# Kernel tuning notes

Measured on AMD Instinct MI355X. Metric: run time of the kernel, lower is better.

The kernel has to match this reference:

```python
import math
import jax, jax.numpy as jnp
import numpy as np

D, H, L, DFF, V = 512, 8, 6, 2048, 32000
B, S = 2, 2048
PAD = 1


def _layernorm(x, g, b, eps=1e-5):
    m = x.mean(-1, keepdims=True)
    v = ((x - m) ** 2).mean(-1, keepdims=True)
    return (x - m) / jnp.sqrt(v + eps) * g + b


def _mha(qx, kx, w, b, mask, h=H):
    # w: [4, D, D] (q,k,v,out), b: [4, D]; mask broadcastable to [B,1,Sq,Sk]
    bs, sq, d = qx.shape
    dk = d // h
    def proj(x, i):
        return (x @ w[i] + b[i]).reshape(bs, -1, h, dk).transpose(0, 2, 1, 3)
    q, k, v = proj(qx, 0), proj(kx, 1), proj(kx, 2)
    scores = jnp.einsum('bhqd,bhkd->bhqk', q, k) / math.sqrt(dk)
    scores = jnp.where(mask, scores, -jnp.inf)
    attn = jax.nn.softmax(scores, axis=-1)
    out = jnp.einsum('bhqk,bhkd->bhqd', attn, v).transpose(0, 2, 1, 3).reshape(bs, sq, d)
    return out @ w[3] + b[3]


def _ff(x, w1, b1, w2, b2):
    return jax.nn.relu(x @ w1 + b1) @ w2 + b2


def _sinusoidal_pe(max_len, d):
    pos = np.arange(max_len)[:, None].astype(np.float64)
    div = np.exp(np.arange(0, d, 2) * (-math.log(10000.0) / d))
    pe = np.zeros((max_len, d), np.float32)
    pe[:, 0::2] = np.sin(pos * div)
    pe[:, 1::2] = np.cos(pos * div)
    return jnp.asarray(pe[None])  # [1, max_len, d]


def setup_inputs() -> dict:
    key = jax.random.key(0)
    ks = iter(jax.random.split(key, 32))
    def w(shape):
        return jax.random.normal(next(ks), shape, jnp.float32) * 0.02
    inp = {
        'src': jax.random.randint(next(ks), (B, S), 2, V),
        'tgt': jax.random.randint(next(ks), (B, S), 2, V),
        'src_emb': w((V, D)),
        'tgt_emb': w((V, D)),
        'pe': _sinusoidal_pe(S, D),
        'enc_attn_w': w((L, 4, D, D)), 'enc_attn_b': jnp.zeros((L, 4, D)),
        'enc_ff_w1': w((L, D, DFF)), 'enc_ff_b1': jnp.zeros((L, DFF)),
        'enc_ff_w2': w((L, DFF, D)), 'enc_ff_b2': jnp.zeros((L, D)),
        'enc_ln_g': jnp.ones((L, 2, D)), 'enc_ln_b': jnp.zeros((L, 2, D)),
        'dec_self_w': w((L, 4, D, D)), 'dec_self_b': jnp.zeros((L, 4, D)),
        'dec_src_w': w((L, 4, D, D)), 'dec_src_b': jnp.zeros((L, 4, D)),
        'dec_ff_w1': w((L, D, DFF)), 'dec_ff_b1': jnp.zeros((L, DFF)),
        'dec_ff_w2': w((L, DFF, D)), 'dec_ff_b2': jnp.zeros((L, D)),
        'dec_ln_g': jnp.ones((L, 3, D)), 'dec_ln_b': jnp.zeros((L, 3, D)),
        'ln_g': jnp.ones((D,)), 'ln_b': jnp.zeros((D,)),
        'fc_w': w((D, V)), 'fc_b': jnp.zeros((V,)),
    }
    return inp


def reference(src, tgt, src_emb, tgt_emb, pe,
              enc_attn_w, enc_attn_b, enc_ff_w1, enc_ff_b1, enc_ff_w2, enc_ff_b2,
              enc_ln_g, enc_ln_b,
              dec_self_w, dec_self_b, dec_src_w, dec_src_b,
              dec_ff_w1, dec_ff_b1, dec_ff_w2, dec_ff_b2, dec_ln_g, dec_ln_b,
              ln_g, ln_b, fc_w, fc_b):
    s_len, t_len = src.shape[1], tgt.shape[1]
    src_mask = (src != PAD)[:, None, None, :]                      # [B,1,1,Ss]
    tril = jnp.tril(jnp.ones((t_len, t_len), bool))
    tgt_mask = (tgt != PAD)[:, None, None, :] & tril[None, None]   # [B,1,St,St]

    x = src_emb[src] + pe[:, :s_len]
    for l in range(L):
        x2 = _layernorm(x, enc_ln_g[l, 0], enc_ln_b[l, 0])
        x = x + _mha(x2, x2, enc_attn_w[l], enc_attn_b[l], src_mask)
        x2 = _layernorm(x, enc_ln_g[l, 1], enc_ln_b[l, 1])
        x = x + _ff(x2, enc_ff_w1[l], enc_ff_b1[l], enc_ff_w2[l], enc_ff_b2[l])
    memory = x

    y = tgt_emb[tgt] + pe[:, :t_len]
    for l in range(L):
        y2 = _layernorm(y, dec_ln_g[l, 0], dec_ln_b[l, 0])
        y = y + _mha(y2, y2, dec_self_w[l], dec_self_b[l], tgt_mask)
        y2 = _layernorm(y, dec_ln_g[l, 1], dec_ln_b[l, 1])
        y = y + _mha(y2, memory, dec_src_w[l], dec_src_b[l], src_mask)
        y2 = _layernorm(y, dec_ln_g[l, 2], dec_ln_b[l, 2])
        y = y + _ff(y2, dec_ff_w1[l], dec_ff_b1[l], dec_ff_w2[l], dec_ff_b2[l])

    return _layernorm(y, ln_g, ln_b) @ fc_w + fc_b  # [B, St, V]
```

## Files before the change

kernel.cpp:

```cpp
#include <hip/hip_runtime.h>
#include <math.h>

#define D_MODEL 512
#define NHEAD   8
#define NLAYER  6
#define DFF_    2048
#define VOCAB   32000
#define BATCH   2
#define SEQ     2048
#define NTOK    (BATCH*SEQ)
#define PAD_ID  1

typedef __attribute__((ext_vector_type(8))) short s16x8;
typedef __attribute__((ext_vector_type(4))) float f32x4;
typedef unsigned short u16;
typedef unsigned int   u32;
typedef unsigned long long u64;

__device__ __forceinline__ u16 f2bf(float x) {
  u32 u = __builtin_bit_cast(u32, x);
  u += 0x7FFFu + ((u >> 16) & 1u);
  return (u16)(u >> 16);
}

__device__ __forceinline__ float exp2i(float x) {
  float r; asm("v_exp_f32 %0, %1" : "=v"(r) : "v"(x)); return r;
}

__device__ __forceinline__ void gload16(const void* g, void* l) {
  __builtin_amdgcn_global_load_lds(
      (const __attribute__((address_space(1))) u32*)g,
      (__attribute__((address_space(3))) u32*)l, 16, 0, 0);
}

#define CEXP 0.1803368802f

__global__ __launch_bounds__(256) void embed_kernel(
    const int* __restrict__ tok, const float* __restrict__ emb,
    const float* __restrict__ pe, float* __restrict__ out)
{
  const int total = NTOK * D_MODEL;
  for (int i = blockIdx.x * 256 + threadIdx.x; i < total; i += gridDim.x * 256) {
    int t = i >> 9;
    int d = i & 511;
    int s = t & (SEQ - 1);
    out[i] = emb[(size_t)tok[t] * D_MODEL + d] + pe[(size_t)s * D_MODEL + d];
  }
}

__global__ __launch_bounds__(64) void padmask_kernel(
    const int* __restrict__ tok, u64* __restrict__ pm)
{
  int b = blockIdx.y, t = blockIdx.x;
  int lane = threadIdx.x;
  u64 m = __ballot(tok[(size_t)b * SEQ + t * 64 + lane] != PAD_ID);
  if (lane == 0) pm[b * (SEQ / 64) + t] = m;
}

__global__ __launch_bounds__(256) void ln_kernel(
    const float* __restrict__ x, const float* __restrict__ g,
    const float* __restrict__ bb, u16* __restrict__ y)
{
  __shared__ float red[8];
  const size_t row = blockIdx.x;
  const float* xr = x + row * D_MODEL;
  u16* yr = y + row * D_MODEL;
  const int t = threadIdx.x;
  float a0 = xr[t], a1 = xr[t + 256];
  float s = a0 + a1;
  #pragma unroll
  for (int o = 32; o > 0; o >>= 1) s += __shfl_down(s, o, 64);
  int wv = t >> 6, ln = t & 63;
  if (ln == 0) red[wv] = s;
  __syncthreads();
  if (t == 0) red[4] = red[0] + red[1] + red[2] + red[3];
  __syncthreads();
  float mean = red[4] * (1.0f / D_MODEL);
  float d0 = a0 - mean, d1 = a1 - mean;
  float vs = d0 * d0 + d1 * d1;
  #pragma unroll
  for (int o = 32; o > 0; o >>= 1) vs += __shfl_down(vs, o, 64);
  if (ln == 0) red[wv] = vs;
  __syncthreads();
  if (t == 0) red[5] = red[0] + red[1] + red[2] + red[3];
  __syncthreads();
  float inv = rsqrtf(red[5] * (1.0f / D_MODEL) + 1e-5f);
  yr[t]       = f2bf(d0 * inv * g[t]       + bb[t]);
  yr[t + 256] = f2bf(d1 * inv * g[t + 256] + bb[t + 256]);
}

__global__ __launch_bounds__(256) void cvtbf_kernel(
    const float* __restrict__ s, u16* __restrict__ d, int n)
{
  int i = (blockIdx.x * 256 + threadIdx.x) * 8;
  if (i >= n) return;
  float4 a = *(const float4*)&s[i];
  float4 b = *(const float4*)&s[i + 4];
  u32 p0 = (u32)f2bf(a.x) | ((u32)f2bf(a.y) << 16);
  u32 p1 = (u32)f2bf(a.z) | ((u32)f2bf(a.w) << 16);
  u32 p2 = (u32)f2bf(b.x) | ((u32)f2bf(b.y) << 16);
  u32 p3 = (u32)f2bf(b.z) | ((u32)f2bf(b.w) << 16);
  uint4 o; o.x = p0; o.y = p1; o.z = p2; o.w = p3;
  *(uint4*)&d[i] = o;
}

__global__ __launch_bounds__(256) void tconv_kernel(
    const float* __restrict__ src, u16* __restrict__ dst, int K, int N)
{
  __shared__ float tile[64][65];
  const size_t z = blockIdx.z;
  src += z * (size_t)K * N;
  dst += z * (size_t)K * N;
  const int n0 = blockIdx.x * 64, k0 = blockIdx.y * 64;
  const int t = threadIdx.x;
  const int cr = t >> 4, cc = (t & 15) * 4;
  #pragma unroll
  for (int it = 0; it < 4; ++it) {
    int kr = cr + it * 16;
    float4 v = *(const float4*)&src[(size_t)(k0 + kr) * N + n0 + cc];
    tile[kr][cc] = v.x; tile[kr][cc + 1] = v.y; tile[kr][cc + 2] = v.z; tile[kr][cc + 3] = v.w;
  }
  __syncthreads();
  #pragma unroll
  for (int it = 0; it < 4; ++it) {
    int nr = cr + it * 16;
    u32 lo = (u32)f2bf(tile[cc + 0][nr]) | ((u32)f2bf(tile[cc + 1][nr]) << 16);
    u32 hi = (u32)f2bf(tile[cc + 2][nr]) | ((u32)f2bf(tile[cc + 3][nr]) << 16);
    uint2 pk; pk.x = lo; pk.y = hi;
    *(uint2*)&dst[(size_t)(n0 + nr) * K + k0 + cc] = pk;
  }
}

__global__ __launch_bounds__(256) void vtrans_kernel(
    const u16* __restrict__ v, u16* __restrict__ vt)
{
  __shared__ u16 tile[64][65];
  const int bh = blockIdx.z, s0 = blockIdx.x * 64;
  const int b = bh >> 3, h = bh & 7;
  const int t = threadIdx.x;
  const int lr = t >> 3, lc = (t & 7) * 8;
  #pragma unroll
  for (int it = 0; it < 2; ++it) {
    int srow = lr + it * 32;
    s16x8 val = *(const s16x8*)(v + (size_t)(b * SEQ + s0 + srow) * D_MODEL + h * 64 + lc);
    #pragma unroll
    for (int j = 0; j < 8; ++j) tile[srow][lc + j] = (u16)val[j];
  }
  __syncthreads();
  #pragma unroll
  for (int it = 0; it < 2; ++it) {
    int drow = lr + it * 32;
    s16x8 o;
    #pragma unroll
    for (int j = 0; j < 8; ++j) o[j] = (short)tile[lc + j][drow];
    *(s16x8*)(vt + ((size_t)bh * 64 + drow) * SEQ + s0 + lc) = o;
  }
}

template<int MODE, int BM>
__global__ __launch_bounds__(256, 2) void mm_kernel(
    const u16* __restrict__ A, const u16* __restrict__ Wt,
    const float* __restrict__ bias, const float* __restrict__ res,
    void* __restrict__ Cout, int M, int N, int K,
    long long wStride, long long bStride, long long cStride)
{
  constexpr int MI = BM / 32;
  __shared__ u16 As[BM * 64];
  __shared__ u16 Bs[128 * 64];
  const int z = blockIdx.z;
  Wt   += (size_t)z * wStride;
  bias += (size_t)z * bStride;
  const int bm = blockIdx.y * BM, bn = blockIdx.x * 128;
  const int tid = threadIdx.x, lane = tid & 63, w = tid >> 6;
  const int wm = w >> 1, wn = w & 1;
  const int l15 = lane & 15, l4 = lane >> 4;
  const int wrow0 = wm * (BM / 2);
  const u16* aBase = A  + (size_t)bm * K;
  const u16* bBase = Wt + (size_t)bn * K;
  f32x4 acc[MI][4] = {};

  for (int k0 = 0; k0 < K; k0 += 64) {
    #pragma unroll
    for (int i = 0; i < BM / 32; ++i) {
      int lin = i * 256 + tid;
      int r = lin >> 3, sp = lin & 7;
      gload16(aBase + (size_t)r * K + k0 + ((sp ^ (r & 7)) * 8), &As[(i * 256 + w * 64) * 8]);
    }
    #pragma unroll
    for (int i = 0; i < 4; ++i) {
      int lin = i * 256 + tid;
      int r = lin >> 3, sp = lin & 7;
      gload16(bBase + (size_t)r * K + k0 + ((sp ^ (r & 7)) * 8), &Bs[(i * 256 + w * 64) * 8]);
    }
    __syncthreads();
    #pragma unroll
    for (int ks = 0; ks < 2; ++ks) {
      s16x8 af[MI], bf[4];
      #pragma unroll
      for (int mi = 0; mi < MI; ++mi) {
        int rr = wrow0 + mi * 16 + l15;
        af[mi] = *(const s16x8*)&As[(rr << 6) + (((ks * 4 + l4) ^ (rr & 7)) << 3)];
      }
      #pragma unroll
      for (int ni = 0; ni < 4; ++ni) {
        int rr = wn * 64 + ni * 16 + l15;
        bf[ni] = *(const s16x8*)&Bs[(rr << 6) + (((ks * 4 + l4) ^ (rr & 7)) << 3)];
      }
      #pragma unroll
      for (int mi = 0; mi < MI; ++mi)
        #pragma unroll
        for (int ni = 0; ni < 4; ++ni)
          acc[mi][ni] = __builtin_amdgcn_mfma_f32_16x16x32_bf16(af[mi], bf[ni], acc[mi][ni], 0, 0, 0);
    }
    __syncthreads();
  }

  #pragma unroll
  for (int ni = 0; ni < 4; ++ni) {
    int col = bn + wn * 64 + ni * 16 + l15;
    float bb = bias[col];
    #pragma unroll
    for (int mi = 0; mi < MI; ++mi) {
      #pragma unroll
      for (int r = 0; r < 4; ++r) {
        int row = bm + wrow0 + mi * 16 + l4 * 4 + r;
        size_t off = (size_t)z * cStride + (size_t)row * N + col;
        float v = acc[mi][ni][r] + bb;
        if (MODE == 1) v += res[(size_t)row * N + col];
        if (MODE == 3) v = fmaxf(v, 0.0f);
        if (MODE <= 1) ((float*)Cout)[off] = v;
        else           ((u16*)Cout)[off] = f2bf(v);
      }
    }
  }
}

template<int CAUSAL>
__global__ __launch_bounds__(256, 2) void fattn_kernel(
    const u16* __restrict__ Qg, const u16* __restrict__ Kg,
    const u16* __restrict__ Vt, const u64* __restrict__ padm,
    u16* __restrict__ Og)
{
  __shared__ u16 Ks[2][128 * 64];
  __shared__ u16 Vs[2][64 * 128];
  __shared__ u16 Ps[4][16 * 128];
  const int qtile = CAUSAL ? (int)(gridDim.x - 1 - blockIdx.x) : (int)blockIdx.x;
  const int qt = qtile * 64;
  const int h = blockIdx.y, b = blockIdx.z;
  const int tid = threadIdx.x, lane = tid & 63, w = tid >> 6;
  const int l15 = lane & 15, l4 = lane >> 4;
  const int hoff = h * 64;
  const u16* Kbase = Kg + (size_t)(b * SEQ) * D_MODEL + hoff;
  const u16* Vbase = Vt + (size_t)(b * NHEAD + h) * 64 * SEQ;
  const u64* pmb = padm + b * (SEQ / 64);

  s16x8 aq[2];
  {
    const u16* qp = Qg + (size_t)(b * SEQ + qt + w * 16 + l15) * D_MODEL + hoff + l4 * 8;
    aq[0] = *(const s16x8*)qp;
    aq[1] = *(const s16x8*)(qp + 32);
  }

  f32x4 oacc[4] = {};
  float mrow[4] = {-1e30f, -1e30f, -1e30f, -1e30f};
  float lrow[4] = {0.f, 0.f, 0.f, 0.f};
  const int nt = CAUSAL ? (qt >> 7) + 1 : SEQ / 128;

  #define STAGE(KV0, BUF)                                                              \
    {                                                                                  \
      _Pragma("unroll")                                                                \
      for (int it = 0; it < 4; ++it) {                                                 \
        int lin = it * 256 + tid;                                                      \
        int rr = lin >> 3, sp = lin & 7;                                               \
        gload16(Kbase + (size_t)((KV0) + rr) * D_MODEL + ((sp ^ (rr & 7)) * 8),        \
                &Ks[BUF][(it * 256 + w * 64) * 8]);                                    \
      }                                                                                \
      _Pragma("unroll")                                                                \
      for (int it = 0; it < 4; ++it) {                                                 \
        int lin = it * 256 + tid;                                                      \
        int rr = lin >> 4, ko = lin & 15;                                              \
        gload16(Vbase + (size_t)rr * SEQ + (KV0) + ((ko ^ (rr & 15)) * 8),             \
                &Vs[BUF][(it * 256 + w * 64) * 8]);                                    \
      }                                                                                \
    }

  STAGE(0, 0);
  __syncthreads();

  for (int kt = 0; kt < nt; ++kt) {
    const int kv0 = kt * 128;
    const int cur = kt & 1;
    if (kt + 1 < nt) STAGE(kv0 + 128, cur ^ 1);

    f32x4 sac[8] = {};
    #pragma unroll
    for (int ks = 0; ks < 2; ++ks)
      #pragma unroll
      for (int jn = 0; jn < 8; ++jn) {
        int rr = jn * 16 + l15;
        s16x8 bk = *(const s16x8*)&Ks[cur][(rr << 6) + (((ks * 4 + l4) ^ (rr & 7)) << 3)];
        sac[jn] = __builtin_amdgcn_mfma_f32_16x16x32_bf16(aq[ks], bk, sac[jn], 0, 0, 0);
      }

    const u64 m0 = pmb[(kv0 >> 6)];
    const u64 m1 = pmb[(kv0 >> 6) + 1];
    const bool lastC = CAUSAL && (kt == nt - 1);
    if (((m0 & m1) != ~0ull) || lastC) {
      #pragma unroll
      for (int jn = 0; jn < 8; ++jn) {
        int kvg = kv0 + jn * 16 + l15;
        u64 mm = (jn < 4) ? m0 : m1;
        bool okp = (mm >> ((jn & 3) * 16 + l15)) & 1;
        #pragma unroll
        for (int r = 0; r < 4; ++r) {
          int qg = qt + w * 16 + l4 * 4 + r;
          bool ok = okp && (!CAUSAL || kvg <= qg);
          if (!ok) sac[jn][r] = -1e30f;
        }
      }
    }

    float mx[4];
    #pragma unroll
    for (int r = 0; r < 4; ++r) {
      float m = fmaxf(fmaxf(fmaxf(sac[0][r], sac[1][r]), fmaxf(sac[2][r], sac[3][r])),
                      fmaxf(fmaxf(sac[4][r], sac[5][r]), fmaxf(sac[6][r], sac[7][r])));
      #pragma unroll
      for (int o = 1; o < 16; o <<= 1) m = fmaxf(m, __shfl_xor(m, o, 16));
      mx[r] = m;
    }
    float growth = fmaxf(fmaxf(mx[0] - mrow[0], mx[1] - mrow[1]),
                         fmaxf(mx[2] - mrow[2], mx[3] - mrow[3]));
    if (__any(growth > 64.0f)) {
      #pragma unroll
      for (int r = 0; r < 4; ++r) {
        float mn = fmaxf(mrow[r], mx[r]);
        float sc = exp2i((mrow[r] - mn) * CEXP);
        mrow[r] = mn;
        lrow[r] *= sc;
        #pragma unroll
        for (int jn = 0; jn < 4; ++jn) oacc[jn][r] *= sc;
      }
    }

    #pragma unroll
    for (int r = 0; r < 4; ++r) {
      const int prow = l4 * 4 + r;
      float rs = 0.f;
      #pragma unroll
      for (int jn = 0; jn < 8; ++jn) {
        float pv = exp2i((sac[jn][r] - mrow[r]) * CEXP);
        rs += pv;
        int g = ((jn * 2 + (l15 >> 3)) ^ prow) & 15;
        Ps[w][prow * 128 + g * 8 + (l15 & 7)] = f2bf(pv);
      }
      #pragma unroll
      for (int o = 1; o < 16; o <<= 1) rs += __shfl_xor(rs, o, 16);
      lrow[r] += rs;
    }

    #pragma unroll
    for (int kslot = 0; kslot < 4; ++kslot) {
      s16x8 pa = *(const s16x8*)&Ps[w][l15 * 128 + ((((kslot * 4 + l4) ^ l15) & 15) << 3)];
      #pragma unroll
      for (int jn = 0; jn < 4; ++jn) {
        int rr = jn * 16 + l15;
        s16x8 bv = *(const s16x8*)&Vs[cur][(rr << 7) + (((kslot * 4 + l4) ^ (rr & 15)) << 3)];
        oacc[jn] = __builtin_amdgcn_mfma_f32_16x16x32_bf16(pa, bv, oacc[jn], 0, 0, 0);
      }
    }
    __syncthreads();
  }
  #undef STAGE

  float inv[4];
  #pragma unroll
  for (int r = 0; r < 4; ++r) inv[r] = 1.0f / lrow[r];
  #pragma unroll
  for (int jn = 0; jn < 4; ++jn)
    #pragma unroll
    for (int r = 0; r < 4; ++r)
      Og[(size_t)(b * SEQ + qt + w * 16 + l4 * 4 + r) * D_MODEL + hoff + jn * 16 + l15] =
          f2bf(oacc[jn][r] * inv[r]);
}

extern "C" void kernel_launch(void* const* d_in, const int* in_sizes, int n_in,
                              void* d_out, int out_size, void* d_ws, size_t ws_size,
                              hipStream_t stream)
{
  const int*   src        = (const int*)  d_in[0];
  const int*   tgt        = (const int*)  d_in[1];
  const float* src_emb    = (const float*)d_in[2];
  const float* tgt_emb    = (const float*)d_in[3];
  const float* pe         = (const float*)d_in[4];
  const float* enc_attn_w = (const float*)d_in[5];
  const float* enc_attn_b = (const float*)d_in[6];
  const float* enc_ff_w1  = (const float*)d_in[7];
  const float* enc_ff_b1  = (const float*)d_in[8];
  const float* enc_ff_w2  = (const float*)d_in[9];
  const float* enc_ff_b2  = (const float*)d_in[10];
  const float* enc_ln_g   = (const float*)d_in[11];
  const float* enc_ln_bb  = (const float*)d_in[12];
  const float* dec_self_w = (const float*)d_in[13];
  const float* dec_self_b = (const float*)d_in[14];
  const float* dec_src_w  = (const float*)d_in[15];
  const float* dec_src_b  = (const float*)d_in[16];
  const float* dec_ff_w1  = (const float*)d_in[17];
  const float* dec_ff_b1  = (const float*)d_in[18];
  const float* dec_ff_w2  = (const float*)d_in[19];
  const float* dec_ff_b2  = (const float*)d_in[20];
  const float* dec_ln_g   = (const float*)d_in[21];
  const float* dec_ln_bb  = (const float*)d_in[22];
  const float* fin_ln_g   = (const float*)d_in[23];
  const float* fin_ln_b   = (const float*)d_in[24];
  const float* fc_w       = (const float*)d_in[25];
  const float* fc_b       = (const float*)d_in[26];
  float* out = (float*)d_out;

  const size_t DD = (size_t)D_MODEL * D_MODEL;
  const size_t FD = (size_t)D_MODEL * DFF_;
  const size_t TD = (size_t)NTOK * D_MODEL;

  char* ob = (char*)d_out;
  size_t off = 0;
  auto alloco = [&](size_t bytes) { void* p = ob + off; off += (bytes + 255) & ~(size_t)255; return p; };
  u16* wt_enc_attn = (u16*)alloco(24 * DD * 2);
  u16* wt_dec_self = (u16*)alloco(24 * DD * 2);
  u16* wt_dec_src  = (u16*)alloco(24 * DD * 2);
  u16* wt_enc_ff1  = (u16*)alloco(6 * FD * 2);
  u16* wt_enc_ff2  = (u16*)alloco(6 * FD * 2);
  u16* wt_dec_ff1  = (u16*)alloco(6 * FD * 2);
  u16* wt_dec_ff2  = (u16*)alloco(6 * FD * 2);
  u16* qb   = (u16*)alloco(3 * TD * 2);
  u16* kb   = qb + TD;
  u16* vb   = kb + TD;
  u16* vtb  = (u16*)alloco(TD * 2);
  u16* aob  = (u16*)alloco(TD * 2);
  u16* hbb  = (u16*)alloco((size_t)NTOK * DFF_ * 2);
  u16* memb = (u16*)alloco(TD * 2);

  char* wsb = (char*)d_ws;
  u16*   fcwt = (u16*)wsb;
  size_t wo = ((size_t)VOCAB * D_MODEL * 2 + 255) & ~(size_t)255;
  float* xe  = (float*)(wsb + wo); wo += TD * 4;
  float* yd  = (float*)(wsb + wo); wo += TD * 4;
  u16*   x2b = (u16*)(wsb + wo);   wo += TD * 2;
  u64*   pmS = (u64*)(wsb + wo);   wo += 1024;
  u64*   pmT = (u64*)(wsb + wo);

  dim3 blk(256);
  dim3 gP64(4, 64, 1), gQKV(4, 64, 3), gKV(4, 64, 2);
  dim3 gFF1(16, 32, 1), gFF2(4, 64, 1), gFC(250, 32, 1);
  dim3 gAttn(SEQ / 64, NHEAD, BATCH);
  dim3 gVT(SEQ / 64, 1, BATCH * NHEAD);
  dim3 gPM(SEQ / 64, BATCH);
  const long long llDD = (long long)DD, llTD = (long long)TD;

  padmask_kernel<<<gPM, dim3(64), 0, stream>>>(src, pmS);
  padmask_kernel<<<gPM, dim3(64), 0, stream>>>(tgt, pmT);
  tconv_kernel<<<dim3(8, 8, 24), blk, 0, stream>>>(enc_attn_w, wt_enc_attn, 512, 512);
  tconv_kernel<<<dim3(8, 8, 24), blk, 0, stream>>>(dec_self_w, wt_dec_self, 512, 512);
  tconv_kernel<<<dim3(8, 8, 24), blk, 0, stream>>>(dec_src_w,  wt_dec_src,  512, 512);
  tconv_kernel<<<dim3(32, 8, 6), blk, 0, stream>>>(enc_ff_w1, wt_enc_ff1, 512, 2048);
  tconv_kernel<<<dim3(8, 32, 6), blk, 0, stream>>>(enc_ff_w2, wt_enc_ff2, 2048, 512);
  tconv_kernel<<<dim3(32, 8, 6), blk, 0, stream>>>(dec_ff_w1, wt_dec_ff1, 512, 2048);
  tconv_kernel<<<dim3(8, 32, 6), blk, 0, stream>>>(dec_ff_w2, wt_dec_ff2, 2048, 512);
  tconv_kernel<<<dim3(500, 8, 1), blk, 0, stream>>>(fc_w, fcwt, 512, VOCAB);

  embed_kernel<<<dim3(2048), blk, 0, stream>>>(src, src_emb, pe, xe);
  for (int l = 0; l < NLAYER; ++l) {
    ln_kernel<<<dim3(NTOK), blk, 0, stream>>>(xe, enc_ln_g + (size_t)(l * 2 + 0) * D_MODEL,
                                              enc_ln_bb + (size_t)(l * 2 + 0) * D_MODEL, x2b);
    mm_kernel<2, 64><<<gQKV, blk, 0, stream>>>(x2b, wt_enc_attn + (size_t)l * 4 * DD,
        enc_attn_b + (size_t)l * 4 * D_MODEL, nullptr, qb, NTOK, 512, 512, llDD, D_MODEL, llTD);
    vtrans_kernel<<<gVT, blk, 0, stream>>>(vb, vtb);
    fattn_kernel<0><<<gAttn, blk, 0, stream>>>(qb, kb, vtb, pmS, aob);
    mm_kernel<1, 64><<<gP64, blk, 0, stream>>>(aob, wt_enc_attn + (size_t)(l * 4 + 3) * DD,
        enc_attn_b + (size_t)(l * 4 + 3) * D_MODEL, xe, xe, NTOK, 512, 512, 0, 0, 0);
    ln_kernel<<<dim3(NTOK), blk, 0, stream>>>(xe, enc_ln_g + (size_t)(l * 2 + 1) * D_MODEL,
                                              enc_ln_bb + (size_t)(l * 2 + 1) * D_MODEL, x2b);
    mm_kernel<3, 128><<<gFF1, blk, 0, stream>>>(x2b, wt_enc_ff1 + (size_t)l * FD,
        enc_ff_b1 + (size_t)l * DFF_, nullptr, hbb, NTOK, DFF_, 512, 0, 0, 0);
    mm_kernel<1, 64><<<gFF2, blk, 0, stream>>>(hbb, wt_enc_ff2 + (size_t)l * FD,
        enc_ff_b2 + (size_t)l * D_MODEL, xe, xe, NTOK, 512, DFF_, 0, 0, 0);
  }
  cvtbf_kernel<<<dim3(1024), blk, 0, stream>>>(xe, memb, NTOK * D_MODEL);

  embed_kernel<<<dim3(2048), blk, 0, stream>>>(tgt, tgt_emb, pe, yd);
  for (int l = 0; l < NLAYER; ++l) {
    const u16* Ws = wt_dec_self + (size_t)l * 4 * DD;
    const u16* Wc = wt_dec_src + (size_t)l * 4 * DD;
    const float* bs  = dec_self_b + (size_t)l * 4 * D_MODEL;
    const float* bcb = dec_src_b + (size_t)l * 4 * D_MODEL;
    ln_kernel<<<dim3(NTOK), blk, 0, stream>>>(yd, dec_ln_g + (size_t)(l * 3 + 0) * D_MODEL,
                                              dec_ln_bb + (size_t)(l * 3 + 0) * D_MODEL, x2b);
    mm_kernel<2, 64><<<gQKV, blk, 0, stream>>>(x2b, Ws, bs, nullptr, qb, NTOK, 512, 512, llDD, D_MODEL, llTD);
    vtrans_kernel<<<gVT, blk, 0, stream>>>(vb, vtb);
    fattn_kernel<1><<<gAttn, blk, 0, stream>>>(qb, kb, vtb, pmT, aob);
    mm_kernel<1, 64><<<gP64, blk, 0, stream>>>(aob, Ws + 3 * DD, bs + 3 * D_MODEL, yd, yd,
                                               NTOK, 512, 512, 0, 0, 0);
    ln_kernel<<<dim3(NTOK), blk, 0, stream>>>(yd, dec_ln_g + (size_t)(l * 3 + 1) * D_MODEL,
                                              dec_ln_bb + (size_t)(l * 3 + 1) * D_MODEL, x2b);
    mm_kernel<2, 64><<<gP64, blk, 0, stream>>>(x2b, Wc, bcb, nullptr, qb, NTOK, 512, 512, 0, 0, 0);
    mm_kernel<2, 64><<<gKV, blk, 0, stream>>>(memb, Wc + DD, bcb + D_MODEL, nullptr, kb,
                                              NTOK, 512, 512, llDD, D_MODEL, llTD);
    vtrans_kernel<<<gVT, blk, 0, stream>>>(vb, vtb);
    fattn_kernel<0><<<gAttn, blk, 0, stream>>>(qb, kb, vtb, pmS, aob);
    mm_kernel<1, 64><<<gP64, blk, 0, stream>>>(aob, Wc + 3 * DD, bcb + 3 * D_MODEL, yd, yd,
                                               NTOK, 512, 512, 0, 0, 0);
    ln_kernel<<<dim3(NTOK), blk, 0, stream>>>(yd, dec_ln_g + (size_t)(l * 3 + 2) * D_MODEL,
                                              dec_ln_bb + (size_t)(l * 3 + 2) * D_MODEL, x2b);
    mm_kernel<3, 128><<<gFF1, blk, 0, stream>>>(x2b, wt_dec_ff1 + (size_t)l * FD,
        dec_ff_b1 + (size_t)l * DFF_, nullptr, hbb, NTOK, DFF_, 512, 0, 0, 0);
    mm_kernel<1, 64><<<gFF2, blk, 0, stream>>>(hbb, wt_dec_ff2 + (size_t)l * FD,
        dec_ff_b2 + (size_t)l * D_MODEL, yd, yd, NTOK, 512, DFF_, 0, 0, 0);
  }

  ln_kernel<<<dim3(NTOK), blk, 0, stream>>>(yd, fin_ln_g, fin_ln_b, x2b);
  mm_kernel<0, 128><<<gFC, blk, 0, stream>>>(x2b, fcwt, fc_b, nullptr, out, NTOK, VOCAB, 512, 0, 0, 0);

  (void)in_sizes; (void)n_in; (void)out_size; (void)ws_size;
}
```

Baseline: 2.690 ms.

## Fuse V transpose into GEMM epilogue, batch cross-attn KV, narrow N tiles

The V projection GEMM now writes V already transposed through a shared-memory tile in its epilogue, so the separate vtrans kernel and its round trip through global memory go away. The decoder cross-attention K/V projections of encoder memory for all six layers run as one batched launch right after the encoder, instead of one launch per layer. The GEMM gains a BN template parameter, and the N=512 GEMMs switch to 64-wide tiles to put more blocks on the device. This adds 12*TD of buffers for the cached K/V, and the smaller tiles reduce per-block data reuse.

```diff
diff --git a/kernel.cpp b/kernel.cpp
--- a/kernel.cpp
+++ b/kernel.cpp
@@ -131,53 +131,38 @@
   }
 }
 
-__global__ __launch_bounds__(256) void vtrans_kernel(
-    const u16* __restrict__ v, u16* __restrict__ vt)
-{
-  __shared__ u16 tile[64][65];
-  const int bh = blockIdx.z, s0 = blockIdx.x * 64;
-  const int b = bh >> 3, h = bh & 7;
-  const int t = threadIdx.x;
-  const int lr = t >> 3, lc = (t & 7) * 8;
-  #pragma unroll
-  for (int it = 0; it < 2; ++it) {
-    int srow = lr + it * 32;
-    s16x8 val = *(const s16x8*)(v + (size_t)(b * SEQ + s0 + srow) * D_MODEL + h * 64 + lc);
-    #pragma unroll
-    for (int j = 0; j < 8; ++j) tile[srow][lc + j] = (u16)val[j];
-  }
-  __syncthreads();
-  #pragma unroll
-  for (int it = 0; it < 2; ++it) {
-    int drow = lr + it * 32;
-    s16x8 o;
-    #pragma unroll
-    for (int j = 0; j < 8; ++j) o[j] = (short)tile[lc + j][drow];
-    *(s16x8*)(vt + ((size_t)bh * 64 + drow) * SEQ + s0 + lc) = o;
-  }
-}
-
-template<int MODE, int BM>
+template<int MODE, int BM, int BN, int MAP>
 __global__ __launch_bounds__(256, 2) void mm_kernel(
     const u16* __restrict__ A, const u16* __restrict__ Wt,
     const float* __restrict__ bias, const float* __restrict__ res,
-    void* __restrict__ Cout, int M, int N, int K,
+    void* __restrict__ Cout, u16* __restrict__ vtOut,
+    int M, int N, int K,
     long long wStride, long long bStride, long long cStride)
 {
   constexpr int MI = BM / 32;
-  __shared__ u16 As[BM * 64];
-  __shared__ u16 Bs[128 * 64];
+  constexpr int NI = BN / 32;
+  __shared__ u16 sh[(BM + BN) * 64];
+  u16* As = sh;
+  u16* Bs = sh + BM * 64;
   const int z = blockIdx.z;
-  Wt   += (size_t)z * wStride;
-  bias += (size_t)z * bStride;
-  const int bm = blockIdx.y * BM, bn = blockIdx.x * 128;
+  size_t wOff, bOff;
+  if (MAP == 1) {
+    wOff = (size_t)(z >> 1) * 4 * 262144 + (size_t)(1 + (z & 1)) * 262144;
+    bOff = (size_t)(z >> 1) * 4 * 512 + (size_t)(1 + (z & 1)) * 512;
+  } else {
+    wOff = (size_t)z * wStride;
+    bOff = (size_t)z * bStride;
+  }
+  Wt += wOff;
+  bias += bOff;
+  const int bm = blockIdx.y * BM, bn = blockIdx.x * BN;
   const int tid = threadIdx.x, lane = tid & 63, w = tid >> 6;
   const int wm = w >> 1, wn = w & 1;
   const int l15 = lane & 15, l4 = lane >> 4;
-  const int wrow0 = wm * (BM / 2);
+  const int wrow0 = wm * (BM / 2), wcol0 = wn * (BN / 2);
   const u16* aBase = A  + (size_t)bm * K;
   const u16* bBase = Wt + (size_t)bn * K;
-  f32x4 acc[MI][4] = {};
+  f32x4 acc[MI][NI] = {};
 
   for (int k0 = 0; k0 < K; k0 += 64) {
     #pragma unroll
@@ -187,7 +172,7 @@
       gload16(aBase + (size_t)r * K + k0 + ((sp ^ (r & 7)) * 8), &As[(i * 256 + w * 64) * 8]);
     }
     #pragma unroll
-    for (int i = 0; i < 4; ++i) {
+    for (int i = 0; i < BN / 32; ++i) {
       int lin = i * 256 + tid;
       int r = lin >> 3, sp = lin & 7;
       gload16(bBase + (size_t)r * K + k0 + ((sp ^ (r & 7)) * 8), &Bs[(i * 256 + w * 64) * 8]);
@@ -195,36 +180,63 @@
     __syncthreads();
     #pragma unroll
     for (int ks = 0; ks < 2; ++ks) {
-      s16x8 af[MI], bf[4];
+      s16x8 af[MI], bf[NI];
       #pragma unroll
       for (int mi = 0; mi < MI; ++mi) {
         int rr = wrow0 + mi * 16 + l15;
         af[mi] = *(const s16x8*)&As[(rr << 6) + (((ks * 4 + l4) ^ (rr & 7)) << 3)];
       }
       #pragma unroll
-      for (int ni = 0; ni < 4; ++ni) {
-        int rr = wn * 64 + ni * 16 + l15;
+      for (int ni = 0; ni < NI; ++ni) {
+        int rr = wcol0 + ni * 16 + l15;
         bf[ni] = *(const s16x8*)&Bs[(rr << 6) + (((ks * 4 + l4) ^ (rr & 7)) << 3)];
       }
       #pragma unroll
       for (int mi = 0; mi < MI; ++mi)
         #pragma unroll
-        for (int ni = 0; ni < 4; ++ni)
+        for (int ni = 0; ni < NI; ++ni)
           acc[mi][ni] = __builtin_amdgcn_mfma_f32_16x16x32_bf16(af[mi], bf[ni], acc[mi][ni], 0, 0, 0);
     }
     __syncthreads();
   }
 
-  #pragma unroll
-  for (int ni = 0; ni < 4; ++ni) {
-    int col = bn + wn * 64 + ni * 16 + l15;
+  const bool vpath = (MODE == 4 && z == 2) || (MODE == 5 && (z & 1) == 1);
+  if (vpath) {
+    u16* TT = sh;
+    #pragma unroll
+    for (int mi = 0; mi < MI; ++mi)
+      #pragma unroll
+      for (int ni = 0; ni < NI; ++ni)
+        #pragma unroll
+        for (int r = 0; r < 4; ++r) {
+          int rowl = wrow0 + mi * 16 + l4 * 4 + r;
+          int coll = wcol0 + ni * 16 + l15;
+          TT[coll * 72 + rowl] = f2bf(acc[mi][ni][r] + bias[bn + coll]);
+        }
+    __syncthreads();
+    const int b = bm >> 11, s0loc = bm & 2047, h = bn >> 6;
+    const int layer = (MODE == 5) ? (z >> 1) : 0;
+    u16* vbase = vtOut + (size_t)layer * ((size_t)NTOK * D_MODEL)
+               + ((size_t)(b * NHEAD + h) * 64) * SEQ;
+    int d = tid >> 2, sc = (tid & 3) * 16;
+    s16x8 v0 = *(const s16x8*)&TT[d * 72 + sc];
+    s16x8 v1 = *(const s16x8*)&TT[d * 72 + sc + 8];
+    *(s16x8*)(vbase + (size_t)d * SEQ + s0loc + sc) = v0;
+    *(s16x8*)(vbase + (size_t)d * SEQ + s0loc + sc + 8) = v1;
+    return;
+  }
+
+  const int zi = (MAP == 1) ? (z >> 1) : z;
+  #pragma unroll
+  for (int ni = 0; ni < NI; ++ni) {
+    int col = bn + wcol0 + ni * 16 + l15;
     float bb = bias[col];
     #pragma unroll
     for (int mi = 0; mi < MI; ++mi) {
       #pragma unroll
       for (int r = 0; r < 4; ++r) {
         int row = bm + wrow0 + mi * 16 + l4 * 4 + r;
-        size_t off = (size_t)z * cStride + (size_t)row * N + col;
+        size_t off = (size_t)zi * cStride + (size_t)row * N + col;
         float v = acc[mi][ni][r] + bb;
         if (MODE == 1) v += res[(size_t)row * N + col];
         if (MODE == 3) v = fmaxf(v, 0.0f);
@@ -431,13 +443,14 @@
   u16* wt_enc_ff2  = (u16*)alloco(6 * FD * 2);
   u16* wt_dec_ff1  = (u16*)alloco(6 * FD * 2);
   u16* wt_dec_ff2  = (u16*)alloco(6 * FD * 2);
-  u16* qb   = (u16*)alloco(3 * TD * 2);
+  u16* qb   = (u16*)alloco(2 * TD * 2);
   u16* kb   = qb + TD;
-  u16* vb   = kb + TD;
   u16* vtb  = (u16*)alloco(TD * 2);
   u16* aob  = (u16*)alloco(TD * 2);
   u16* hbb  = (u16*)alloco((size_t)NTOK * DFF_ * 2);
   u16* memb = (u16*)alloco(TD * 2);
+  u16* ckb  = (u16*)alloco(6 * TD * 2);
+  u16* cvtb = (u16*)alloco(6 * TD * 2);
 
   char* wsb = (char*)d_ws;
   u16*   fcwt = (u16*)wsb;
@@ -449,10 +462,9 @@
   u64*   pmT = (u64*)(wsb + wo);
 
   dim3 blk(256);
-  dim3 gP64(4, 64, 1), gQKV(4, 64, 3), gKV(4, 64, 2);
-  dim3 gFF1(16, 32, 1), gFF2(4, 64, 1), gFC(250, 32, 1);
+  dim3 gN512(8, 64, 1), gQKV(8, 64, 3), gCKV(8, 64, 12);
+  dim3 gFF1(16, 32, 1), gFF2(8, 64, 1), gFC(250, 32, 1);
   dim3 gAttn(SEQ / 64, NHEAD, BATCH);
-  dim3 gVT(SEQ / 64, 1, BATCH * NHEAD);
   dim3 gPM(SEQ / 64, BATCH);
   const long long llDD = (long long)DD, llTD = (long long)TD;
 
@@ -471,20 +483,22 @@
   for (int l = 0; l < NLAYER; ++l) {
     ln_kernel<<<dim3(NTOK), blk, 0, stream>>>(xe, enc_ln_g + (size_t)(l * 2 + 0) * D_MODEL,
                                               enc_ln_bb + (size_t)(l * 2 + 0) * D_MODEL, x2b);
-    mm_kernel<2, 64><<<gQKV, blk, 0, stream>>>(x2b, wt_enc_attn + (size_t)l * 4 * DD,
-        enc_attn_b + (size_t)l * 4 * D_MODEL, nullptr, qb, NTOK, 512, 512, llDD, D_MODEL, llTD);
-    vtrans_kernel<<<gVT, blk, 0, stream>>>(vb, vtb);
+    mm_kernel<4, 64, 64, 0><<<gQKV, blk, 0, stream>>>(x2b, wt_enc_attn + (size_t)l * 4 * DD,
+        enc_attn_b + (size_t)l * 4 * D_MODEL, nullptr, qb, vtb, NTOK, 512, 512, llDD, D_MODEL, llTD);
     fattn_kernel<0><<<gAttn, blk, 0, stream>>>(qb, kb, vtb, pmS, aob);
-    mm_kernel<1, 64><<<gP64, blk, 0, stream>>>(aob, wt_enc_attn + (size_t)(l * 4 + 3) * DD,
-        enc_attn_b + (size_t)(l * 4 + 3) * D_MODEL, xe, xe, NTOK, 512, 512, 0, 0, 0);
+    mm_kernel<1, 64, 64, 0><<<gN512, blk, 0, stream>>>(aob, wt_enc_attn + (size_t)(l * 4 + 3) * DD,
+        enc_attn_b + (size_t)(l * 4 + 3) * D_MODEL, xe, xe, nullptr, NTOK, 512, 512, 0, 0, 0);
     ln_kernel<<<dim3(NTOK), blk, 0, stream>>>(xe, enc_ln_g + (size_t)(l * 2 + 1) * D_MODEL,
                                               enc_ln_bb + (size_t)(l * 2 + 1) * D_MODEL, x2b);
-    mm_kernel<3, 128><<<gFF1, blk, 0, stream>>>(x2b, wt_enc_ff1 + (size_t)l * FD,
-        enc_ff_b1 + (size_t)l * DFF_, nullptr, hbb, NTOK, DFF_, 512, 0, 0, 0);
-    mm_kernel<1, 64><<<gFF2, blk, 0, stream>>>(hbb, wt_enc_ff2 + (size_t)l * FD,
-        enc_ff_b2 + (size_t)l * D_MODEL, xe, xe, NTOK, 512, DFF_, 0, 0, 0);
+    mm_kernel<3, 128, 128, 0><<<gFF1, blk, 0, stream>>>(x2b, wt_enc_ff1 + (size_t)l * FD,
+        enc_ff_b1 + (size_t)l * DFF_, nullptr, hbb, nullptr, NTOK, DFF_, 512, 0, 0, 0);
+    mm_kernel<1, 64, 64, 0><<<gFF2, blk, 0, stream>>>(hbb, wt_enc_ff2 + (size_t)l * FD,
+        enc_ff_b2 + (size_t)l * D_MODEL, xe, xe, nullptr, NTOK, 512, DFF_, 0, 0, 0);
   }
   cvtbf_kernel<<<dim3(1024), blk, 0, stream>>>(xe, memb, NTOK * D_MODEL);
+
+  mm_kernel<5, 64, 64, 1><<<gCKV, blk, 0, stream>>>(memb, wt_dec_src, dec_src_b, nullptr,
+      ckb, cvtb, NTOK, 512, 512, 0, 0, llTD);
 
   embed_kernel<<<dim3(2048), blk, 0, stream>>>(tgt, tgt_emb, pe, yd);
   for (int l = 0; l < NLAYER; ++l) {
@@ -494,30 +508,30 @@
     const float* bcb = dec_src_b + (size_t)l * 4 * D_MODEL;
     ln_kernel<<<dim3(NTOK), blk, 0, stream>>>(yd, dec_ln_g + (size_t)(l * 3 + 0) * D_MODEL,
                                               dec_ln_bb + (size_t)(l * 3 + 0) * D_MODEL, x2b);
-    mm_kernel<2, 64><<<gQKV, blk, 0, stream>>>(x2b, Ws, bs, nullptr, qb, NTOK, 512, 512, llDD, D_MODEL, llTD);
-    vtrans_kernel<<<gVT, blk, 0, stream>>>(vb, vtb);
+    mm_kernel<4, 64, 64, 0><<<gQKV, blk, 0, stream>>>(x2b, Ws, bs, nullptr, qb, vtb,
+                                                      NTOK, 512, 512, llDD, D_MODEL, llTD);
     fattn_kernel<1><<<gAttn, blk, 0, stream>>>(qb, kb, vtb, pmT, aob);
-    mm_kernel<1, 64><<<gP64, blk, 0, stream>>>(aob, Ws + 3 * DD, bs + 3 * D_MODEL, yd, yd,
-                                               NTOK, 512, 512, 0, 0, 0);
+    mm_kernel<1, 64, 64, 0><<<gN512, blk, 0, stream>>>(aob, Ws + 3 * DD, bs + 3 * D_MODEL, yd, yd,
+                                                       nullptr, NTOK, 512, 512, 0, 0, 0);
     ln_kernel<<<dim3(NTOK), blk, 0, stream>>>(yd, dec_ln_g + (size_t)(l * 3 + 1) * D_MODEL,
                                               dec_ln_bb + (size_t)(l * 3 + 1) * D_MODEL, x2b);
-    mm_kernel<2, 64><<<gP64, blk, 0, stream>>>(x2b, Wc, bcb, nullptr, qb, NTOK, 512, 512, 0, 0, 0);
-    mm_kernel<2, 64><<<gKV, blk, 0, stream>>>(memb, Wc + DD, bcb + D_MODEL, nullptr, kb,
-                                              NTOK, 512, 512, llDD, D_MODEL, llTD);
-    vtrans_kernel<<<gVT, blk, 0, stream>>>(vb, vtb);
-    fattn_kernel<0><<<gAttn, blk, 0, stream>>>(qb, kb, vtb, pmS, aob);
-    mm_kernel<1, 64><<<gP64, blk, 0, stream>>>(aob, Wc + 3 * DD, bcb + 3 * D_MODEL, yd, yd,
-                                               NTOK, 512, 512, 0, 0, 0);
+    mm_kernel<2, 64, 64, 0><<<gN512, blk, 0, stream>>>(x2b, Wc, bcb, nullptr, qb, nullptr,
+                                                       NTOK, 512, 512, 0, 0, 0);
+    fattn_kernel<0><<<gAttn, blk, 0, stream>>>(qb, ckb + (size_t)l * TD, cvtb + (size_t)l * TD,
+                                               pmS, aob);
+    mm_kernel<1, 64, 64, 0><<<gN512, blk, 0, stream>>>(aob, Wc + 3 * DD, bcb + 3 * D_MODEL, yd, yd,
+                                                       nullptr, NTOK, 512, 512, 0, 0, 0);
     ln_kernel<<<dim3(NTOK), blk, 0, stream>>>(yd, dec_ln_g + (size_t)(l * 3 + 2) * D_MODEL,
                                               dec_ln_bb + (size_t)(l * 3 + 2) * D_MODEL, x2b);
-    mm_kernel<3, 128><<<gFF1, blk, 0, stream>>>(x2b, wt_dec_ff1 + (size_t)l * FD,
-        dec_ff_b1 + (size_t)l * DFF_, nullptr, hbb, NTOK, DFF_, 512, 0, 0, 0);
-    mm_kernel<1, 64><<<gFF2, blk, 0, stream>>>(hbb, wt_dec_ff2 + (size_t)l * FD,
-        dec_ff_b2 + (size_t)l * D_MODEL, yd, yd, NTOK, 512, DFF_, 0, 0, 0);
+    mm_kernel<3, 128, 128, 0><<<gFF1, blk, 0, stream>>>(x2b, wt_dec_ff1 + (size_t)l * FD,
+        dec_ff_b1 + (size_t)l * DFF_, nullptr, hbb, nullptr, NTOK, DFF_, 512, 0, 0, 0);
+    mm_kernel<1, 64, 64, 0><<<gFF2, blk, 0, stream>>>(hbb, wt_dec_ff2 + (size_t)l * FD,
+        dec_ff_b2 + (size_t)l * D_MODEL, yd, yd, nullptr, NTOK, 512, DFF_, 0, 0, 0);
   }
 
   ln_kernel<<<dim3(NTOK), blk, 0, stream>>>(yd, fin_ln_g, fin_ln_b, x2b);
-  mm_kernel<0, 128><<<gFC, blk, 0, stream>>>(x2b, fcwt, fc_b, nullptr, out, NTOK, VOCAB, 512, 0, 0, 0);
+  mm_kernel<0, 128, 128, 0><<<gFC, blk, 0, stream>>>(x2b, fcwt, fc_b, nullptr, out, nullptr,
+                                                     NTOK, VOCAB, 512, 0, 0, 0);
 
   (void)in_sizes; (void)n_in; (void)out_size; (void)ws_size;
 }
```

New measurement: 2.516 ms. -6.5%, faster.
